# Kernel optimization log

Hardware: AMD Instinct MI355X
Metric: run time of the kernel (lower is better)

## Reference

```python
import jax, jax.numpy as jnp
import numpy as np

B, S, D, H, KS, VS, O = 4, 2048, 1024, 16, 64, 64, 1024


def setup_inputs() -> dict:
    key = jax.random.key(0)
    ks = jax.random.split(key, 11)
    def w(k, shp):
        return jax.random.normal(k, shp, dtype=jnp.float32) * 0.02
    return {
        "Q": jax.random.normal(ks[0], (B, S, D), dtype=jnp.float32),
        "K": jax.random.normal(ks[1], (B, S, D), dtype=jnp.float32),
        "V": jax.random.normal(ks[2], (B, S, D), dtype=jnp.float32),
        # per-head projection weights stacked over heads (equivalent to 3*H separate nn.Linear)
        "Wq": w(ks[3], (H, D, KS)), "bq": w(ks[4], (H, KS)),
        "Wk": w(ks[5], (H, D, KS)), "bk": w(ks[6], (H, KS)),
        "Wv": w(ks[7], (H, D, VS)), "bv": w(ks[8], (H, VS)),
        "Wo": w(ks[9], (H * VS, O)), "bo": w(ks[10], (O,)),
    }


def reference(Q, K, V, Wq, bq, Wk, bk, Wv, bv, Wo, bo):
    scale = jnp.sqrt(jnp.asarray(KS, dtype=Q.dtype))
    # per-head linear projections (vectorized over heads)
    q = jnp.einsum('bsd,hdk->bhsk', Q, Wq) + bq[:, None, :]   # [B,H,S,KS]
    k = jnp.einsum('bsd,hdk->bhsk', K, Wk) + bk[:, None, :]   # [B,H,S,KS]
    v = jnp.einsum('bsd,hdv->bhsv', V, Wv) + bv[:, None, :]   # [B,H,S,VS]
    # scaled dot-product attention, full S x S scores per head
    scores = jnp.einsum('bhsk,bhtk->bhst', q, k) / scale       # [B,H,S,S]
    attn = jax.nn.softmax(scores, axis=-1)
    heads = jnp.einsum('bhst,bhtv->bhsv', attn, v)             # [B,H,S,VS]
    # concat heads along feature dim -> [B,S,H*VS]
    cat = jnp.transpose(heads, (0, 2, 1, 3)).reshape(B, S, H * VS)
    return cat @ Wo + bo
```

## Files before the change

### kernel.cpp

```cpp
#include <hip/hip_runtime.h>
#include <hip/hip_fp16.h>
#include <cstdint>
#include <cstddef>

typedef _Float16 f16;
typedef _Float16 f16x8 __attribute__((ext_vector_type(8)));
typedef _Float16 f16x4 __attribute__((ext_vector_type(4)));
typedef float    f32x4 __attribute__((ext_vector_type(4)));

#define MFMA(a, b, c) __builtin_amdgcn_mfma_f32_16x16x32_f16(a, b, c, 0, 0, 0)


__device__ __forceinline__ void gload_lds16(const f16* g, f16* l) {
    __builtin_amdgcn_global_load_lds(
        (const __attribute__((address_space(1))) void*)g,
        (__attribute__((address_space(3))) void*)l, 16, 0, 0);
}

__global__ void k_convert3(const float* __restrict__ Q, const float* __restrict__ K,
                           const float* __restrict__ V, f16* __restrict__ Qh,
                           f16* __restrict__ Kh, f16* __restrict__ Vh) {
    const int seg = blockIdx.x >> 11;
    const int lb  = blockIdx.x & 2047;
    const float* src = seg == 0 ? Q : (seg == 1 ? K : V);
    f16* dst = seg == 0 ? Qh : (seg == 1 ? Kh : Vh);
    int i = lb * blockDim.x + threadIdx.x;
    for (; i < 2097152; i += 524288) {
        float4 v = ((const float4*)src)[i];
        f16x4 h;
        h[0] = (f16)v.x; h[1] = (f16)v.y; h[2] = (f16)v.z; h[3] = (f16)v.w;
        ((f16x4*)dst)[i] = h;
    }
}

__global__ void k_transpose_all(const float* __restrict__ Wq, const float* __restrict__ Wk,
                                const float* __restrict__ Wv, const float* __restrict__ Wo,
                                f16* __restrict__ WT, f16* __restrict__ WoT) {
    __shared__ float T[64][65];
    const int bx = blockIdx.x;
    const int widx = bx >> 8, sub = bx & 255;
    const int nb = sub >> 4, db = sub & 15;
    const int tid = threadIdx.x;
    const float* W = widx == 0 ? Wq : (widx == 1 ? Wk : (widx == 2 ? Wv : Wo));
    f16* Wt = (widx < 3) ? (WT + (size_t)widx * 1048576) : WoT;
    const float* src = (widx < 3) ? (W + nb * 65536 + db * 4096)
                                  : (W + db * 65536 + nb * 64);
    const int rstride = (widx < 3) ? 64 : 1024;
    {
        int nn = tid & 63, d0 = tid >> 6;
#pragma unroll
        for (int p = 0; p < 16; ++p) {
            int dd = p * 4 + d0;
            T[dd][nn] = src[dd * rstride + nn];
        }
    }
    __syncthreads();
    {
        int dd = tid & 63, n0 = tid >> 6;
#pragma unroll
        for (int p = 0; p < 16; ++p) {
            int nn = p * 4 + n0;
            Wt[(size_t)(nb * 64 + nn) * 1024 + db * 64 + dd] = (f16)T[dd][nn];
        }
    }
}

__global__ __launch_bounds__(256) void k_gemm_qkv(
    const f16* __restrict__ Qh, const f16* __restrict__ Kh, const f16* __restrict__ Vh,
    const f16* __restrict__ WT, const float* __restrict__ bq,
    const float* __restrict__ bk, const float* __restrict__ bv,
    f16* __restrict__ qout, f16* __restrict__ kout, f16* __restrict__ vout, float SC) {
    __shared__ f16 As[128 * 32];
    __shared__ f16 Bs[128 * 32];
    const int yy = blockIdx.y;
    const int seg = yy >> 3;
    const f16* A    = seg == 0 ? Qh : (seg == 1 ? Kh : Vh);
    const f16* Bt   = WT + (size_t)seg * 1048576;
    const float* bias = seg == 0 ? bq : (seg == 1 ? bk : bv);
    const float scale = seg == 0 ? SC : 1.0f;

    const int tid = threadIdx.x;
    const int wid = tid >> 6, lane = tid & 63;
    const int wr = wid >> 1, wc = wid & 1;
    const int lr = lane & 15, lg = lane >> 4;
    const int row0 = blockIdx.x * 128, col0 = (yy & 7) * 128;

    f32x4 acc[4][4];
#pragma unroll
    for (int m = 0; m < 4; ++m)
#pragma unroll
        for (int n = 0; n < 4; ++n) acc[m][n] = (f32x4){0.f, 0.f, 0.f, 0.f};

    const int c0 = tid, c1 = tid + 256;
    const int r0 = c0 >> 2, cb0 = (c0 & 3) * 8;
    const int r1 = c1 >> 2, cb1 = (c1 & 3) * 8;

    for (int k0 = 0; k0 < 1024; k0 += 32) {
        __syncthreads();
        gload_lds16(&A[(size_t)(row0 + r0) * 1024 + k0 + cb0], &As[c0 * 8]);
        gload_lds16(&Bt[(size_t)(col0 + r0) * 1024 + k0 + cb0], &Bs[c0 * 8]);
        gload_lds16(&A[(size_t)(row0 + r1) * 1024 + k0 + cb1], &As[c1 * 8]);
        gload_lds16(&Bt[(size_t)(col0 + r1) * 1024 + k0 + cb1], &Bs[c1 * 8]);
        __syncthreads();
        f16x8 af[4], bf[4];
#pragma unroll
        for (int m = 0; m < 4; ++m) af[m] = *(const f16x8*)&As[(wr * 64 + m * 16 + lr) * 32 + lg * 8];
#pragma unroll
        for (int n = 0; n < 4; ++n) bf[n] = *(const f16x8*)&Bs[(wc * 64 + n * 16 + lr) * 32 + lg * 8];
#pragma unroll
        for (int m = 0; m < 4; ++m)
#pragma unroll
            for (int n = 0; n < 4; ++n) acc[m][n] = MFMA(af[m], bf[n], acc[m][n]);
    }

#pragma unroll
    for (int m = 0; m < 4; ++m) {
#pragma unroll
        for (int n = 0; n < 4; ++n) {
            int col = col0 + wc * 64 + n * 16 + lr;
            float bv_ = bias[col];
            int rowb = row0 + wr * 64 + m * 16 + lg * 4;
            int srow = rowb & 2047;
            if (seg == 0) {
#pragma unroll
                for (int r = 0; r < 4; ++r) {
                    int row = rowb + r;
                    size_t a = ((size_t)((row >> 11) * 16 + (col >> 6)) * 2048 + (row & 2047)) * 64 + (col & 63);
                    qout[a] = (f16)((acc[m][n][r] + bv_) * scale);
                }
            } else if (seg == 1) {
                int ks5 = srow & 31;
                int p0 = ((ks5 >> 2) & 1) * 16 + (ks5 >> 3) * 4 + (ks5 & 3);
                size_t abase = (size_t)((rowb >> 11) * 16 + (col >> 6)) * 131072
                             + (size_t)(srow >> 5) * 2048
                             + (size_t)(p0 >> 4) * 512
                             + (size_t)((col & 63) >> 5) * 1024
                             + (size_t)((col & 31) >> 3) * 128
                             + (col & 7);
#pragma unroll
                for (int r = 0; r < 4; ++r)
                    kout[abase + (size_t)((p0 & 15) + r) * 8] = (f16)(acc[m][n][r] + bv_);
            } else {
                size_t a = (size_t)((rowb >> 11) * 16 + (col >> 6)) * 131072
                         + (size_t)(srow >> 5) * 2048
                         + (size_t)((col & 63) >> 4) * 512
                         + (size_t)((srow & 31) >> 3) * 128
                         + (size_t)(col & 15) * 8
                         + (srow & 7);
                f16x4 ov;
#pragma unroll
                for (int r = 0; r < 4; ++r) ov[r] = (f16)(acc[m][n][r] + bv_);
                *(f16x4*)&vout[a] = ov;
            }
        }
    }
}

__global__ __launch_bounds__(256) void k_gemm_out(const f16* __restrict__ A,
                                                  const f16* __restrict__ Bt,
                                                  const float* __restrict__ bias,
                                                  float* __restrict__ Cout) {
    __shared__ f16 As[128 * 32];
    __shared__ f16 Bs[128 * 32];
    const int tid = threadIdx.x;
    const int wid = tid >> 6, lane = tid & 63;
    const int wr = wid >> 1, wc = wid & 1;
    const int lr = lane & 15, lg = lane >> 4;
    const int row0 = blockIdx.x * 128, col0 = blockIdx.y * 128;

    f32x4 acc[4][4];
#pragma unroll
    for (int m = 0; m < 4; ++m)
#pragma unroll
        for (int n = 0; n < 4; ++n) acc[m][n] = (f32x4){0.f, 0.f, 0.f, 0.f};

    const int c0 = tid, c1 = tid + 256;
    const int r0 = c0 >> 2, cb0 = (c0 & 3) * 8;
    const int r1 = c1 >> 2, cb1 = (c1 & 3) * 8;

    for (int k0 = 0; k0 < 1024; k0 += 32) {
        __syncthreads();
        gload_lds16(&A[(size_t)(row0 + r0) * 1024 + k0 + cb0], &As[c0 * 8]);
        gload_lds16(&Bt[(size_t)(col0 + r0) * 1024 + k0 + cb0], &Bs[c0 * 8]);
        gload_lds16(&A[(size_t)(row0 + r1) * 1024 + k0 + cb1], &As[c1 * 8]);
        gload_lds16(&Bt[(size_t)(col0 + r1) * 1024 + k0 + cb1], &Bs[c1 * 8]);
        __syncthreads();
        f16x8 af[4], bf[4];
#pragma unroll
        for (int m = 0; m < 4; ++m) af[m] = *(const f16x8*)&As[(wr * 64 + m * 16 + lr) * 32 + lg * 8];
#pragma unroll
        for (int n = 0; n < 4; ++n) bf[n] = *(const f16x8*)&Bs[(wc * 64 + n * 16 + lr) * 32 + lg * 8];
#pragma unroll
        for (int m = 0; m < 4; ++m)
#pragma unroll
            for (int n = 0; n < 4; ++n) acc[m][n] = MFMA(af[m], bf[n], acc[m][n]);
    }

#pragma unroll
    for (int m = 0; m < 4; ++m) {
#pragma unroll
        for (int n = 0; n < 4; ++n) {
            int col = col0 + wc * 64 + n * 16 + lr;
            float bv = bias[col];
#pragma unroll
            for (int r = 0; r < 4; ++r) {
                int row = row0 + wr * 64 + m * 16 + lg * 4 + r;
                Cout[(size_t)row * 1024 + col] = acc[m][n][r] + bv;
            }
        }
    }
}

#define ATTN_TILE(Kc, Vc)                                                     \
    do {                                                                      \
        f16x8 ka0 = *(const f16x8*)&(Kc)[fo];                                 \
        f16x8 ka1 = *(const f16x8*)&(Kc)[fo + 1024];                          \
        f16x8 ka2 = *(const f16x8*)&(Kc)[fo + 512];                           \
        f16x8 ka3 = *(const f16x8*)&(Kc)[fo + 1536];                          \
        f32x4 st[2][2];                                                       \
        _Pragma("unroll")                                                     \
        for (int qt = 0; qt < 2; ++qt) {                                      \
            float nm = -m_r[qt];                                              \
            f32x4 z = (f32x4){nm, nm, nm, nm};                                \
            z = MFMA(ka0, qf[qt][0], z);                                      \
            z = MFMA(ka1, qf[qt][1], z);                                      \
            st[qt][0] = z;                                                    \
            f32x4 z2 = (f32x4){nm, nm, nm, nm};                               \
            z2 = MFMA(ka2, qf[qt][0], z2);                                    \
            z2 = MFMA(ka3, qf[qt][1], z2);                                    \
            st[qt][1] = z2;                                                   \
        }                                                                     \
        f16x8 vv0 = *(const f16x8*)&(Vc)[fo];                                 \
        f16x8 vv1 = *(const f16x8*)&(Vc)[fo + 512];                           \
        f16x8 vv2 = *(const f16x8*)&(Vc)[fo + 1024];                          \
        f16x8 vv3 = *(const f16x8*)&(Vc)[fo + 1536];                          \
        {                                                                     \
            float lm[2];                                                      \
            _Pragma("unroll")                                                 \
            for (int qt = 0; qt < 2; ++qt) {                                  \
                float a0 = fmaxf(fmaxf(st[qt][0][0], st[qt][0][1]), st[qt][0][2]); \
                float b0 = fmaxf(fmaxf(st[qt][0][3], st[qt][1][0]), st[qt][1][1]); \
                float c0 = fmaxf(fmaxf(st[qt][1][2], st[qt][1][3]), a0);      \
                lm[qt] = fmaxf(b0, c0);                                       \
            }                                                                 \
            if (__any((lm[0] > THR) || (lm[1] > THR))) {                      \
                _Pragma("unroll")                                             \
                for (int qt = 0; qt < 2; ++qt) {                              \
                    float t0 = lm[qt];                                        \
                    t0 = fmaxf(t0, __shfl_xor(t0, 16, 64));                   \
                    t0 = fmaxf(t0, __shfl_xor(t0, 32, 64));                   \
                    float delta = fmaxf(0.f, t0);                             \
                    float alpha = __builtin_amdgcn_exp2f(-delta);             \
                    _Pragma("unroll")                                         \
                    for (int m = 0; m < 4; ++m)                               \
                        _Pragma("unroll")                                     \
                        for (int r = 0; r < 4; ++r) o[qt][m][r] *= alpha;     \
                    l_p[qt] *= alpha;                                         \
                    m_r[qt] += delta;                                         \
                    _Pragma("unroll")                                         \
                    for (int t = 0; t < 2; ++t)                               \
                        _Pragma("unroll")                                     \
                        for (int r = 0; r < 4; ++r) st[qt][t][r] -= delta;    \
                }                                                             \
            }                                                                 \
        }                                                                     \
        f16x8 pf[2];                                                          \
        _Pragma("unroll")                                                     \
        for (int qt = 0; qt < 2; ++qt) {                                      \
            float ps = 0.f;                                                   \
            union { uint32_t u[4]; f16x8 v; } bb;                             \
            _Pragma("unroll")                                                 \
            for (int t = 0; t < 2; ++t)                                       \
                _Pragma("unroll")                                             \
                for (int pr = 0; pr < 2; ++pr) {                              \
                    float e0 = __builtin_amdgcn_exp2f(st[qt][t][2 * pr]);     \
                    float e1 = __builtin_amdgcn_exp2f(st[qt][t][2 * pr + 1]); \
                    ps += e0 + e1;                                            \
                    auto hp = __builtin_amdgcn_cvt_pkrtz(e0, e1);             \
                    bb.u[t * 2 + pr] = __builtin_bit_cast(uint32_t, hp);      \
                }                                                             \
            l_p[qt] += ps;                                                    \
            pf[qt] = bb.v;                                                    \
        }                                                                     \
        _Pragma("unroll")                                                     \
        for (int qt = 0; qt < 2; ++qt) {                                      \
            o[qt][0] = MFMA(vv0, pf[qt], o[qt][0]);                           \
            o[qt][1] = MFMA(vv1, pf[qt], o[qt][1]);                           \
            o[qt][2] = MFMA(vv2, pf[qt], o[qt][2]);                           \
            o[qt][3] = MFMA(vv3, pf[qt], o[qt][3]);                           \
        }                                                                     \
    } while (0)

__global__ __launch_bounds__(256, 4) void k_attn(const f16* __restrict__ q,
                                                 const f16* __restrict__ k2,
                                                 const f16* __restrict__ v2,
                                                 f16* __restrict__ cat) {
    const int g = blockIdx.x;
    const int xcd = g & 7, i = g >> 3;
    const int bh = xcd * 8 + (i >> 4);
    const int qb = i & 15;
    const int b = bh >> 4, h = bh & 15;

    const int tid = threadIdx.x, wid = tid >> 6, lane = tid & 63;
    const int lr = lane & 15, lg = lane >> 4;
    const int qw = qb * 128 + wid * 32;

    __shared__ f16 Ks[4][2048];
    __shared__ f16 Vs[4][2048];

    const float THR = 8.0f;

    f16x8 qf[2][2];
#pragma unroll
    for (int qt = 0; qt < 2; ++qt)
#pragma unroll
        for (int hf = 0; hf < 2; ++hf)
            qf[qt][hf] = *(const f16x8*)&q[((size_t)bh * 2048 + qw + qt * 16 + lr) * 64 + hf * 32 + lg * 8];

    const f16* kt = k2 + (size_t)bh * 131072;
    const f16* vt = v2 + (size_t)bh * 131072;
    const int so = tid * 8;
    const int fo = lane * 8;

    f32x4 o[2][4];
#pragma unroll
    for (int qt = 0; qt < 2; ++qt)
#pragma unroll
        for (int m = 0; m < 4; ++m) o[qt][m] = (f32x4){0.f, 0.f, 0.f, 0.f};
    float m_r[2] = {0.f, 0.f}, l_p[2] = {0.f, 0.f};

    gload_lds16(kt + so, &Ks[0][so]);
    gload_lds16(vt + so, &Vs[0][so]);
    gload_lds16(kt + 2048 + so, &Ks[1][so]);
    gload_lds16(vt + 2048 + so, &Vs[1][so]);
    __syncthreads();

    for (int pp = 0; pp < 32; ++pp) {
        const int t0 = 2 * pp;
        const int ba = t0 & 3, bb2 = (t0 + 1) & 3;
        const int bc = (t0 + 2) & 3, bd = (t0 + 3) & 3;

        gload_lds16(kt + (size_t)(t0 + 2) * 2048 + so, &Ks[bc][so]);
        gload_lds16(vt + (size_t)(t0 + 2) * 2048 + so, &Vs[bc][so]);
        gload_lds16(kt + (size_t)(t0 + 3) * 2048 + so, &Ks[bd][so]);
        gload_lds16(vt + (size_t)(t0 + 3) * 2048 + so, &Vs[bd][so]);

        ATTN_TILE(&Ks[ba][0], &Vs[ba][0]);
        ATTN_TILE(&Ks[bb2][0], &Vs[bb2][0]);

        __syncthreads();
    }

#pragma unroll
    for (int qt = 0; qt < 2; ++qt) {
        float l = l_p[qt];
        l += __shfl_xor(l, 16, 64);
        l += __shfl_xor(l, 32, 64);
        float inv = 1.f / l;
        size_t cb = ((size_t)b * 2048 + qw + qt * 16 + lr) * 1024 + h * 64 + lg * 4;
#pragma unroll
        for (int m = 0; m < 4; ++m) {
            f16x4 ov;
#pragma unroll
            for (int r = 0; r < 4; ++r) ov[r] = (f16)(o[qt][m][r] * inv);
            *(f16x4*)&cat[cb + m * 16] = ov;
        }
    }
}

extern "C" void kernel_launch(void* const* d_in, const int* in_sizes, int n_in,
                              void* d_out, int out_size, void* d_ws, size_t ws_size,
                              hipStream_t stream) {
    const float* Q  = (const float*)d_in[0];
    const float* K  = (const float*)d_in[1];
    const float* V  = (const float*)d_in[2];
    const float* Wq = (const float*)d_in[3];
    const float* bq = (const float*)d_in[4];
    const float* Wk = (const float*)d_in[5];
    const float* bk = (const float*)d_in[6];
    const float* Wv = (const float*)d_in[7];
    const float* bv = (const float*)d_in[8];
    const float* Wo = (const float*)d_in[9];
    const float* bo = (const float*)d_in[10];

    char* ws = (char*)d_ws;
    size_t off = 0;
    auto alloc = [&](size_t bytes) {
        char* p = ws + off;
        off += (bytes + 255) & ~(size_t)255;
        return p;
    };
    f16* Qh  = (f16*)alloc(8192ULL * 1024 * 2);
    f16* Kh  = (f16*)alloc(8192ULL * 1024 * 2);
    f16* Vh  = (f16*)alloc(8192ULL * 1024 * 2);
    f16* WT  = (f16*)alloc(3ULL * 1024 * 1024 * 2);
    f16* WoT = (f16*)alloc(1024ULL * 1024 * 2);
    f16* qb  = (f16*)alloc(8192ULL * 1024 * 2);
    f16* kb2 = (f16*)alloc(8192ULL * 1024 * 2);
    f16* vb2 = (f16*)alloc(8192ULL * 1024 * 2);
    f16* cat = (f16*)alloc(8192ULL * 1024 * 2);

    k_convert3<<<6144, 256, 0, stream>>>(Q, K, V, Qh, Kh, Vh);
    k_transpose_all<<<1024, 256, 0, stream>>>(Wq, Wk, Wv, Wo, WT, WoT);

    const float SC = 0.125f * 1.44269504089f;
    k_gemm_qkv<<<dim3(64, 24), 256, 0, stream>>>(Qh, Kh, Vh, WT, bq, bk, bv,
                                                 qb, kb2, vb2, SC);

    k_attn<<<1024, 256, 0, stream>>>(qb, kb2, vb2, cat);

    k_gemm_out<<<dim3(64, 8), 256, 0, stream>>>(cat, WoT, bo, (float*)d_out);
}
```

Measured before the change: 211.9 us.

## Triple-buffer projection GEMMs with 256-row tiles and padded LDS

Both projection GEMMs move from 128x128 tiles with a single LDS buffer and two barriers per K step to 256x128 tiles run by 512 threads. Direct global-to-LDS loads go into a three-stage ring with a K step of 64, a partial vmcnt wait and one barrier per step. The LDS rows are padded to 68 units to reduce bank conflicts. This aims to overlap memory latency with MFMA work, but it halves the grid to 768 and 256 blocks. The larger LDS footprint limits each CU to one block, which may hurt latency hiding on the smaller output GEMM.

```diff
diff --git a/kernel.cpp b/kernel.cpp
--- a/kernel.cpp
+++ b/kernel.cpp
@@ -65,13 +65,73 @@
     }
 }
 
-__global__ __launch_bounds__(256) void k_gemm_qkv(
+#define G256_STAGE(AD, BD, ASRC, BSRC, KT)                                      \
+    do {                                                                        \
+        int ktc = (KT);                                                         \
+        _Pragma("unroll")                                                       \
+        for (int i2 = 0; i2 < 4; ++i2) {                                        \
+            int gA = wid * 4 + i2;                       \
+            gload_lds16(&(ASRC)[(size_t)(row0 + gA * 8 + (lane >> 3)) * 1024    \
+                                + ktc * 64 + (lane & 7) * 8],                   \
+                        &(AD)[(gA * 68 + lane) * 8]);                           \
+        }                                                                       \
+        _Pragma("unroll")                                                       \
+        for (int i2 = 0; i2 < 2; ++i2) {                                        \
+            int gB = wid * 2 + i2;                                   \
+            gload_lds16(&(BSRC)[(size_t)(col0 + gB * 8 + (lane >> 3)) * 1024    \
+                                + ktc * 64 + (lane & 7) * 8],                   \
+                        &(BD)[(gB * 68 + lane) * 8]);                           \
+        }                                                                       \
+    } while (0)
+
+#define G256_COMPUTE(AB, BB)                                                    \
+    do {                                                                        \
+        _Pragma("unroll")                                                       \
+        for (int kk = 0; kk < 2; ++kk) {                                        \
+            f16x8 af[4], bf[4];                                                 \
+            _Pragma("unroll")                                                   \
+            for (int m = 0; m < 4; ++m) {                                       \
+                int rw = wm * 64 + m * 16 + lr;                                 \
+                af[m] = *(const f16x8*)&(AB)[((rw >> 3) * 68 + (rw & 7) * 8     \
+                                              + kk * 4 + lg) * 8];              \
+            }                                                                   \
+            _Pragma("unroll")                                                   \
+            for (int n = 0; n < 4; ++n) {                                       \
+                int rw = wn * 64 + n * 16 + lr;                                 \
+                bf[n] = *(const f16x8*)&(BB)[((rw >> 3) * 68 + (rw & 7) * 8     \
+                                              + kk * 4 + lg) * 8];              \
+            }                                                                   \
+            _Pragma("unroll")                                                   \
+            for (int m = 0; m < 4; ++m)                                         \
+                _Pragma("unroll")                                               \
+                for (int n = 0; n < 4; ++n)                                     \
+                    acc[m][n] = MFMA(af[m], bf[n], acc[m][n]);                  \
+        }                                                                       \
+    } while (0)
+
+#define G256_PIPELINE(ASRC, BSRC)                                              \
+    int cur = 0, nx1 = 1, nx2 = 2;                                             \
+    G256_STAGE(As3, Bs3, ASRC, BSRC, 0);                                       \
+    for (int t = 0; t < 16; ++t) {                                             \
+        int tn = t < 15 ? t + 1 : 15;                                          \
+        G256_STAGE(As3 + nx1 * 17408, Bs3 + nx1 * 8704, ASRC, BSRC, tn);       \
+        asm volatile("s_waitcnt vmcnt(6)" ::: "memory");                       \
+        __builtin_amdgcn_sched_barrier(0);                                     \
+        __builtin_amdgcn_s_barrier();                                          \
+        __builtin_amdgcn_sched_barrier(0);                                     \
+        const f16* Ab = As3 + cur * 17408;                                     \
+        const f16* Bb = Bs3 + cur * 8704;                                      \
+        G256_COMPUTE(Ab, Bb);                                                  \
+        int tmp = cur; cur = nx1; nx1 = nx2; nx2 = tmp;                        \
+    }
+
+__global__ __launch_bounds__(512, 1) void k_gemm_qkv256(
     const f16* __restrict__ Qh, const f16* __restrict__ Kh, const f16* __restrict__ Vh,
     const f16* __restrict__ WT, const float* __restrict__ bq,
     const float* __restrict__ bk, const float* __restrict__ bv,
     f16* __restrict__ qout, f16* __restrict__ kout, f16* __restrict__ vout, float SC) {
-    __shared__ f16 As[128 * 32];
-    __shared__ f16 Bs[128 * 32];
+    __shared__ f16 As3[3 * 17408];
+    __shared__ f16 Bs3[3 * 8704];
     const int yy = blockIdx.y;
     const int seg = yy >> 3;
     const f16* A    = seg == 0 ? Qh : (seg == 1 ? Kh : Vh);
@@ -81,9 +141,9 @@
 
     const int tid = threadIdx.x;
     const int wid = tid >> 6, lane = tid & 63;
-    const int wr = wid >> 1, wc = wid & 1;
+    const int wm = wid >> 1, wn = wid & 1;
     const int lr = lane & 15, lg = lane >> 4;
-    const int row0 = blockIdx.x * 128, col0 = (yy & 7) * 128;
+    const int row0 = blockIdx.x * 256, col0 = (yy & 7) * 128;
 
     f32x4 acc[4][4];
 #pragma unroll
@@ -91,35 +151,15 @@
 #pragma unroll
         for (int n = 0; n < 4; ++n) acc[m][n] = (f32x4){0.f, 0.f, 0.f, 0.f};
 
-    const int c0 = tid, c1 = tid + 256;
-    const int r0 = c0 >> 2, cb0 = (c0 & 3) * 8;
-    const int r1 = c1 >> 2, cb1 = (c1 & 3) * 8;
-
-    for (int k0 = 0; k0 < 1024; k0 += 32) {
-        __syncthreads();
-        gload_lds16(&A[(size_t)(row0 + r0) * 1024 + k0 + cb0], &As[c0 * 8]);
-        gload_lds16(&Bt[(size_t)(col0 + r0) * 1024 + k0 + cb0], &Bs[c0 * 8]);
-        gload_lds16(&A[(size_t)(row0 + r1) * 1024 + k0 + cb1], &As[c1 * 8]);
-        gload_lds16(&Bt[(size_t)(col0 + r1) * 1024 + k0 + cb1], &Bs[c1 * 8]);
-        __syncthreads();
-        f16x8 af[4], bf[4];
-#pragma unroll
-        for (int m = 0; m < 4; ++m) af[m] = *(const f16x8*)&As[(wr * 64 + m * 16 + lr) * 32 + lg * 8];
-#pragma unroll
-        for (int n = 0; n < 4; ++n) bf[n] = *(const f16x8*)&Bs[(wc * 64 + n * 16 + lr) * 32 + lg * 8];
-#pragma unroll
-        for (int m = 0; m < 4; ++m)
-#pragma unroll
-            for (int n = 0; n < 4; ++n) acc[m][n] = MFMA(af[m], bf[n], acc[m][n]);
-    }
+    G256_PIPELINE(A, Bt)
 
 #pragma unroll
     for (int m = 0; m < 4; ++m) {
 #pragma unroll
         for (int n = 0; n < 4; ++n) {
-            int col = col0 + wc * 64 + n * 16 + lr;
+            int col = col0 + wn * 64 + n * 16 + lr;
             float bv_ = bias[col];
-            int rowb = row0 + wr * 64 + m * 16 + lg * 4;
+            int rowb = row0 + wm * 64 + m * 16 + lg * 4;
             int srow = rowb & 2047;
             if (seg == 0) {
 #pragma unroll
@@ -156,17 +196,17 @@
     }
 }
 
-__global__ __launch_bounds__(256) void k_gemm_out(const f16* __restrict__ A,
-                                                  const f16* __restrict__ Bt,
-                                                  const float* __restrict__ bias,
-                                                  float* __restrict__ Cout) {
-    __shared__ f16 As[128 * 32];
-    __shared__ f16 Bs[128 * 32];
+__global__ __launch_bounds__(512, 1) void k_gemm_out256(const f16* __restrict__ A,
+                                                        const f16* __restrict__ Bt,
+                                                        const float* __restrict__ bias,
+                                                        float* __restrict__ Cout) {
+    __shared__ f16 As3[3 * 17408];
+    __shared__ f16 Bs3[3 * 8704];
     const int tid = threadIdx.x;
     const int wid = tid >> 6, lane = tid & 63;
-    const int wr = wid >> 1, wc = wid & 1;
+    const int wm = wid >> 1, wn = wid & 1;
     const int lr = lane & 15, lg = lane >> 4;
-    const int row0 = blockIdx.x * 128, col0 = blockIdx.y * 128;
+    const int row0 = blockIdx.x * 256, col0 = blockIdx.y * 128;
 
     f32x4 acc[4][4];
 #pragma unroll
@@ -174,37 +214,17 @@
 #pragma unroll
         for (int n = 0; n < 4; ++n) acc[m][n] = (f32x4){0.f, 0.f, 0.f, 0.f};
 
-    const int c0 = tid, c1 = tid + 256;
-    const int r0 = c0 >> 2, cb0 = (c0 & 3) * 8;
-    const int r1 = c1 >> 2, cb1 = (c1 & 3) * 8;
-
-    for (int k0 = 0; k0 < 1024; k0 += 32) {
-        __syncthreads();
-        gload_lds16(&A[(size_t)(row0 + r0) * 1024 + k0 + cb0], &As[c0 * 8]);
-        gload_lds16(&Bt[(size_t)(col0 + r0) * 1024 + k0 + cb0], &Bs[c0 * 8]);
-        gload_lds16(&A[(size_t)(row0 + r1) * 1024 + k0 + cb1], &As[c1 * 8]);
-        gload_lds16(&Bt[(size_t)(col0 + r1) * 1024 + k0 + cb1], &Bs[c1 * 8]);
-        __syncthreads();
-        f16x8 af[4], bf[4];
-#pragma unroll
-        for (int m = 0; m < 4; ++m) af[m] = *(const f16x8*)&As[(wr * 64 + m * 16 + lr) * 32 + lg * 8];
-#pragma unroll
-        for (int n = 0; n < 4; ++n) bf[n] = *(const f16x8*)&Bs[(wc * 64 + n * 16 + lr) * 32 + lg * 8];
-#pragma unroll
-        for (int m = 0; m < 4; ++m)
-#pragma unroll
-            for (int n = 0; n < 4; ++n) acc[m][n] = MFMA(af[m], bf[n], acc[m][n]);
-    }
+    G256_PIPELINE(A, Bt)
 
 #pragma unroll
     for (int m = 0; m < 4; ++m) {
 #pragma unroll
         for (int n = 0; n < 4; ++n) {
-            int col = col0 + wc * 64 + n * 16 + lr;
+            int col = col0 + wn * 64 + n * 16 + lr;
             float bv = bias[col];
 #pragma unroll
             for (int r = 0; r < 4; ++r) {
-                int row = row0 + wr * 64 + m * 16 + lg * 4 + r;
+                int row = row0 + wm * 64 + m * 16 + lg * 4 + r;
                 Cout[(size_t)row * 1024 + col] = acc[m][n][r] + bv;
             }
         }
@@ -404,10 +424,10 @@
     k_transpose_all<<<1024, 256, 0, stream>>>(Wq, Wk, Wv, Wo, WT, WoT);
 
     const float SC = 0.125f * 1.44269504089f;
-    k_gemm_qkv<<<dim3(64, 24), 256, 0, stream>>>(Qh, Kh, Vh, WT, bq, bk, bv,
-                                                 qb, kb2, vb2, SC);
+    k_gemm_qkv256<<<dim3(32, 24), 512, 0, stream>>>(Qh, Kh, Vh, WT, bq, bk, bv,
+                                                    qb, kb2, vb2, SC);
 
     k_attn<<<1024, 256, 0, stream>>>(qb, kb2, vb2, cat);
 
-    k_gemm_out<<<dim3(64, 8), 256, 0, stream>>>(cat, WoT, bo, (float*)d_out);
-}
+    k_gemm_out256<<<dim3(32, 8), 512, 0, stream>>>(cat, WoT, bo, (float*)d_out);
+}
```

New measurement: 202.9 us. -4.2%, faster.
